# Kernel tuning notes

Measured on AMD Instinct MI355X. Metric: run time of the kernel, lower is better.

Reference implementation:

```python
import jax, jax.numpy as jnp
import numpy as np

NUM_HEADS = 8
HEAD_SPLITS = [2, 3, 3]          # heads per window size
WINDOWS = [3, 5, 7]


def _dwconv(x, w, b, k):
    """Depthwise 2D conv, SAME padding. x:[B,C,H,W], w:[C,1,k,k], b:[C]."""
    p = k // 2
    y = jax.lax.conv_general_dilated(
        x, w, window_strides=(1, 1), padding=[(p, p), (p, p)],
        dimension_numbers=("NCHW", "OIHW", "NCHW"),
        feature_group_count=x.shape[1])
    return y + b[None, :, None, None]


def setup_inputs() -> dict:
    key = jax.random.key(0)
    ks = jax.random.split(key, 8)
    B, N, C = 8, 3137, 768
    c = C // NUM_HEADS  # 96
    inp = {
        "x": jax.random.normal(ks[0], (B, N, C), dtype=jnp.float32),
        "qkv_w": jax.random.normal(ks[1], (3 * C, C), dtype=jnp.float32) * 0.02,
        "qkv_b": jnp.zeros((3 * C,), dtype=jnp.float32),
        "proj_w": jax.random.normal(ks[2], (C, C), dtype=jnp.float32) * 0.02,
        "proj_b": jnp.zeros((C,), dtype=jnp.float32),
        "conv3_w": jax.random.normal(ks[3], (2 * c, 1, 3, 3), dtype=jnp.float32) * 0.02,
        "conv3_b": jnp.zeros((2 * c,), dtype=jnp.float32),
        "conv5_w": jax.random.normal(ks[4], (3 * c, 1, 5, 5), dtype=jnp.float32) * 0.02,
        "conv5_b": jnp.zeros((3 * c,), dtype=jnp.float32),
        "conv7_w": jax.random.normal(ks[5], (3 * c, 1, 7, 7), dtype=jnp.float32) * 0.02,
        "conv7_b": jnp.zeros((3 * c,), dtype=jnp.float32),
        "H": 56,
        "W": 56,
    }
    return inp


def reference(x, qkv_w, qkv_b, proj_w, proj_b,
              conv3_w, conv3_b, conv5_w, conv5_b, conv7_w, conv7_b, H, W):
    B, N, C = x.shape
    h = NUM_HEADS
    c = C // h
    scale = c ** -0.5

    # qkv projection -> q,k,v each [B,h,N,c]
    qkv = x @ qkv_w.T + qkv_b
    qkv = qkv.reshape(B, N, 3, h, c).transpose(2, 0, 3, 1, 4)
    q, k, v = qkv[0], qkv[1], qkv[2]

    # factorized attention: softmax over token axis of k
    k_softmax = jax.nn.softmax(k, axis=2)
    kv = jnp.einsum("bhnc,bhnd->bhcd", k_softmax, v)       # [B,h,c,c]
    factor_att = jnp.einsum("bhnc,bhcd->bhnd", q, kv)      # [B,h,N,c]

    # ConvRelPosEnc on image tokens
    q_img = q[:, :, 1:, :]                                  # [B,h,HW,c]
    v_img = v[:, :, 1:, :]                                  # [B,h,HW,c]
    v_img = v_img.transpose(0, 1, 3, 2).reshape(B, h * c, H, W)
    splits = np.cumsum([s * c for s in HEAD_SPLITS])[:-1].tolist()
    v2, v5, v7 = jnp.split(v_img, splits, axis=1)
    conv_v = jnp.concatenate([
        _dwconv(v2, conv3_w, conv3_b, 3),
        _dwconv(v5, conv5_w, conv5_b, 5),
        _dwconv(v7, conv7_w, conv7_b, 7),
    ], axis=1)                                              # [B,h*c,H,W]
    conv_v = conv_v.reshape(B, h, c, H * W).transpose(0, 1, 3, 2)  # [B,h,HW,c]
    ev = q_img * conv_v
    crpe = jnp.pad(ev, ((0, 0), (0, 0), (1, 0), (0, 0)))    # zero row for cls token

    out = scale * factor_att + crpe                         # [B,h,N,c]
    out = out.transpose(0, 2, 1, 3).reshape(B, N, C)
    out = out @ proj_w.T + proj_b
    return out
```

## Files before the change

### kernel.cpp

```cpp
#include <hip/hip_runtime.h>
#include <hip/hip_bf16.h>


#define BB 8
#define NN 3137
#define HH 8
#define CH 96
#define HW 3136
#define IMG 56
#define MTOK (BB*NN)
#define NCHK 16
#define CTOK 197

typedef __bf16 bf16x8 __attribute__((ext_vector_type(8)));
typedef unsigned short u16x8 __attribute__((ext_vector_type(8)));
typedef unsigned short u16x4 __attribute__((ext_vector_type(4)));
typedef float  f32x4  __attribute__((ext_vector_type(4)));
typedef float  f32x8  __attribute__((ext_vector_type(8)));

__device__ __forceinline__ void gl_lds16(const void* g, void* l) {
    __builtin_amdgcn_global_load_lds(
        (const __attribute__((address_space(1))) unsigned int*)g,
        (__attribute__((address_space(3))) unsigned int*)l, 16, 0, 0);
}

__global__ __launch_bounds__(256) void cvt_bf16(
    const float* __restrict__ in, unsigned short* __restrict__ out, int n8)
{
    const int i = blockIdx.x * 256 + threadIdx.x;
    if (i < n8) {
        const f32x8 v = ((const f32x8*)in)[i];
        ((u16x8*)out)[i] = (u16x8)__builtin_convertvector(v, bf16x8);
    }
}

template<bool OUT_F32>
__global__ __launch_bounds__(256) void gemm_bt(
    const unsigned short* __restrict__ A, int lda,
    const unsigned short* __restrict__ W,
    const float* __restrict__ bias,
    void* __restrict__ Cptr, int ldc,
    int M, int Nd, int K)
{
    __shared__ alignas(16) unsigned short As[128*32];
    __shared__ alignas(16) unsigned short Bs[128*32];
    const int tid  = threadIdx.x;
    const int nwg = gridDim.x * gridDim.y;
    int orig = blockIdx.y * gridDim.x + blockIdx.x;
    const int q8 = nwg >> 3, r8 = nwg & 7;
    const int xcd = orig & 7, off = orig >> 3;
    const int wgid = (xcd < r8 ? xcd*(q8+1) : r8*(q8+1) + (xcd-r8)*q8) + off;
    const int n0   = (wgid % gridDim.x) * 128;
    const int m0   = (wgid / gridDim.x) * 128;
    const int lane = tid & 63;
    const int wave = tid >> 6;
    const int wm   = (wave >> 1) * 64;
    const int wn   = (wave & 1) * 64;
    const int lr   = lane & 15;
    const int quad = lane >> 4;

    const int r0 = tid >> 2, c0 = (tid & 3) * 8;
    const int r1 = r0 + 64;
    int am0 = m0 + r0; if (am0 > M-1) am0 = M-1;
    int am1 = m0 + r1; if (am1 > M-1) am1 = M-1;
    const unsigned short* a0 = A + (size_t)am0*lda + c0;
    const unsigned short* a1 = A + (size_t)am1*lda + c0;
    const unsigned short* w0 = W + (size_t)(n0+r0)*K + c0;
    const unsigned short* w1 = W + (size_t)(n0+r1)*K + c0;
    unsigned short* lA0 = As + tid*8;
    unsigned short* lA1 = As + (tid+256)*8;
    unsigned short* lB0 = Bs + tid*8;
    unsigned short* lB1 = Bs + (tid+256)*8;

    f32x4 acc[4][4] = {};
    for (int k0 = 0; k0 < K; k0 += 32) {
        __syncthreads();
        gl_lds16(a0 + k0, lA0);
        gl_lds16(a1 + k0, lA1);
        gl_lds16(w0 + k0, lB0);
        gl_lds16(w1 + k0, lB1);
        asm volatile("s_waitcnt vmcnt(0)" ::: "memory");
        __syncthreads();
        bf16x8 af[4], bfr[4];
#pragma unroll
        for (int i = 0; i < 4; ++i) {
            af[i]  = *(const bf16x8*)(As + (wm + i*16 + lr)*32 + quad*8);
            bfr[i] = *(const bf16x8*)(Bs + (wn + i*16 + lr)*32 + quad*8);
        }
#pragma unroll
        for (int i = 0; i < 4; ++i)
#pragma unroll
            for (int j = 0; j < 4; ++j)
                acc[i][j] = __builtin_amdgcn_mfma_f32_16x16x32_bf16(bfr[j], af[i], acc[i][j], 0, 0, 0);
    }
#pragma unroll
    for (int i = 0; i < 4; ++i) {
        const int row = m0 + wm + i*16 + lr;
        if (row < M) {
#pragma unroll
            for (int j = 0; j < 4; ++j) {
                const int col = n0 + wn + j*16 + quad*4;
                const f32x4 bv = *(const f32x4*)(bias + col);
                f32x4 v;
#pragma unroll
                for (int r = 0; r < 4; ++r) v[r] = acc[i][j][r] + bv[r];
                if (OUT_F32) {
                    *(f32x4*)&((float*)Cptr)[(size_t)row*ldc + col] = v;
                } else {
                    u16x4 st;
#pragma unroll
                    for (int r = 0; r < 4; ++r)
                        st[r] = __hip_bfloat16_raw(__float2bfloat16(v[r])).x;
                    *(u16x4*)&((__hip_bfloat16*)Cptr)[(size_t)row*ldc + col] = st;
                }
            }
        }
    }
}

__global__ __launch_bounds__(256) void kv_accum(
    const __hip_bfloat16* __restrict__ qkv,
    float* __restrict__ kvp,
    float* __restrict__ spart)
{
    const int bh = blockIdx.x;
    const int chunk = blockIdx.y;
    const int b = bh >> 3, h = bh & 7;
    const int nstart = chunk * CTOK;
    int nend = nstart + CTOK; if (nend > NN) nend = NN;
    __shared__ float krow[16][96], vrow[16][96];
    __shared__ float sacc[192][8];
    const int t = threadIdx.x;

    const int sr = t / 12, sc = (t % 12) * 8;
    const __hip_bfloat16* kb = qkv + (size_t)b*NN*2304 + 768 + h*96;
    const __hip_bfloat16* vb = kb + 768;
    float ssum[8] = {};

    const int ci = (t >> 4) * 6;
    const int di = (t & 15) * 6;
    float acc[6][6] = {};
    for (int n = nstart; n < nend; n += 16) {
        __syncthreads();
        if (t < 192) {
            const int nn = n + sr;
            if (nn < nend) {
                const bf16x8 kr = *(const bf16x8*)(kb + (size_t)nn*2304 + sc);
                const bf16x8 vr = *(const bf16x8*)(vb + (size_t)nn*2304 + sc);
                const f32x8 kf = __builtin_convertvector(kr, f32x8);
                const f32x8 vf = __builtin_convertvector(vr, f32x8);
                f32x8 ke;
#pragma unroll
                for (int j = 0; j < 8; ++j) { ke[j] = __expf(kf[j]); ssum[j] += ke[j]; }
                *(f32x4*)&krow[sr][sc]   = *(const f32x4*)&ke;
                *(f32x4*)&krow[sr][sc+4] = *((const f32x4*)&ke + 1);
                *(f32x4*)&vrow[sr][sc]   = *(const f32x4*)&vf;
                *(f32x4*)&vrow[sr][sc+4] = *((const f32x4*)&vf + 1);
            } else {
                const f32x4 z = {0.f,0.f,0.f,0.f};
                *(f32x4*)&krow[sr][sc] = z; *(f32x4*)&krow[sr][sc+4] = z;
                *(f32x4*)&vrow[sr][sc] = z; *(f32x4*)&vrow[sr][sc+4] = z;
            }
        }
        __syncthreads();
#pragma unroll 4
        for (int r = 0; r < 16; ++r) {
            float kf[6], vf[6];
#pragma unroll
            for (int i = 0; i < 6; ++i) kf[i] = krow[r][ci+i];
#pragma unroll
            for (int j = 0; j < 6; ++j) vf[j] = vrow[r][di+j];
#pragma unroll
            for (int i = 0; i < 6; ++i)
#pragma unroll
                for (int j = 0; j < 6; ++j)
                    acc[i][j] += kf[i] * vf[j];
        }
    }
    float* outp = kvp + (size_t)(chunk*64 + bh)*9216;
#pragma unroll
    for (int i = 0; i < 6; ++i)
#pragma unroll
        for (int j = 0; j < 6; ++j)
            outp[(ci+i)*96 + (di+j)] = acc[i][j];
    if (t < 192) {
#pragma unroll
        for (int j = 0; j < 8; ++j) sacc[t][j] = ssum[j];
    }
    __syncthreads();
    if (t < 96) {
        const int g = t >> 3, e = t & 7;
        float S = 0.f;
#pragma unroll
        for (int m = 0; m < 16; ++m) S += sacc[g + 12*m][e];
        spart[(size_t)(chunk*64 + bh)*96 + t] = S;
    }
}

__global__ __launch_bounds__(256) void kv_prep(
    const float* __restrict__ kvp, const float* __restrict__ spart,
    unsigned short* __restrict__ kvb)
{
    const int bh = blockIdx.x, y = blockIdx.y;
    __shared__ float sinv[24];
    const int t = threadIdx.x;
    const int cbase = y * 24;
    if (t < 24) {
        float S = 0.f;
#pragma unroll
        for (int ch = 0; ch < NCHK; ++ch)
            S += spart[(size_t)(ch*64 + bh)*96 + cbase + t];
        sinv[t] = 1.0f / S;
    }
    __syncthreads();
    unsigned short* dst = kvb + (size_t)bh*19968;
    for (int i = t; i < 2304; i += 256) {
        const int ii = y*2304 + i;
        const int c = ii / 96, d = ii % 96;
        float v = 0.f;
#pragma unroll
        for (int ch = 0; ch < NCHK; ++ch)
            v += kvp[(size_t)(ch*64 + bh)*9216 + ii];
        v *= sinv[c - cbase];
        const __hip_bfloat16 hb = __float2bfloat16(v);
        const float lo = v - __bfloat162float(hb);
        const __hip_bfloat16 lb = __float2bfloat16(lo);
        dst[d*104 + c]        = __hip_bfloat16_raw(hb).x;
        dst[9984 + d*104 + c] = __hip_bfloat16_raw(lb).x;
    }
}

__global__ __launch_bounds__(256) void fatt(
    const __hip_bfloat16* __restrict__ qkv,
    const unsigned short* __restrict__ kvb,
    const __hip_bfloat16* __restrict__ cv,
    __hip_bfloat16* __restrict__ att)
{
    __shared__ alignas(16) unsigned short kvs[2*96*104];
    const int tile = blockIdx.x, h = blockIdx.y, b = blockIdx.z;
    const int t = threadIdx.x, lane = t & 63, wave = t >> 6;
    const int lr = lane & 15, quad = lane >> 4;

    const unsigned short* kg = kvb + (size_t)(b*8 + h)*19968;
#pragma unroll
    for (int s = 0; s < 10; ++s) {
        const int slot = t + s*256;
        if (slot < 2496) gl_lds16(kg + slot*8, kvs + slot*8);
    }

    const int n0 = tile*128 + wave*32;
    const unsigned short* qbu = (const unsigned short*)qkv + (size_t)b*NN*2304 + h*96;
    bf16x8 af[2][3];
#pragma unroll
    for (int i = 0; i < 2; ++i) {
        int n = n0 + i*16 + lr; if (n > NN-1) n = NN-1;
#pragma unroll
        for (int kk = 0; kk < 3; ++kk)
            af[i][kk] = *(const bf16x8*)(qbu + (size_t)n*2304 + kk*32 + quad*8);
    }
    asm volatile("s_waitcnt vmcnt(0)" ::: "memory");
    __syncthreads();

    f32x4 acc[2][6] = {};
#pragma unroll
    for (int j = 0; j < 6; ++j) {
#pragma unroll
        for (int kk = 0; kk < 3; ++kk) {
            const bf16x8 bhh = *(const bf16x8*)(kvs + (j*16 + lr)*104 + kk*32 + quad*8);
            const bf16x8 bll = *(const bf16x8*)(kvs + 9984 + (j*16 + lr)*104 + kk*32 + quad*8);
#pragma unroll
            for (int i = 0; i < 2; ++i) {
                acc[i][j] = __builtin_amdgcn_mfma_f32_16x16x32_bf16(af[i][kk], bhh, acc[i][j], 0, 0, 0);
                acc[i][j] = __builtin_amdgcn_mfma_f32_16x16x32_bf16(af[i][kk], bll, acc[i][j], 0, 0, 0);
            }
        }
    }

    const float scale = 0.10206207261596577f;
    const __hip_bfloat16* qb  = (const __hip_bfloat16*)qbu;
    const __hip_bfloat16* cvb = cv + (size_t)(b*8 + h)*HW*96;
    __hip_bfloat16* ab = att + (size_t)b*NN*2304 + h*96;
#pragma unroll
    for (int i = 0; i < 2; ++i) {
#pragma unroll
        for (int j = 0; j < 6; ++j) {
            const int col = j*16 + lr;
#pragma unroll
            for (int r = 0; r < 4; ++r) {
                const int n = n0 + i*16 + quad*4 + r;
                if (n < NN) {
                    float v = scale * acc[i][j][r];
                    if (n > 0) {
                        const float qv = __bfloat162float(qb[(size_t)n*2304 + col]);
                        v += qv * __bfloat162float(cvb[(size_t)(n-1)*96 + col]);
                    }
                    ab[(size_t)n*2304 + col] = __float2bfloat16(v);
                }
            }
        }
    }
}

template<int KS>
__device__ __forceinline__ void dw_band(
    float (*vt)[64][36],
    const __hip_bfloat16* __restrict__ vbase,
    const float* __restrict__ wp, float bv,
    __hip_bfloat16* __restrict__ cvo,
    int y0)
{
    constexpr int P = KS/2;
    const int t = threadIdx.x;
    float wr[KS*KS];
#pragma unroll
    for (int i = 0; i < KS*KS; ++i) wr[i] = wp[i];

    const int spx = t >> 2, sc0 = (t & 3) * 8;
    const int ch = t & 31, xs = t >> 5;
    const int xbase = xs*7 + 4 - P;

#pragma unroll
    for (int r = -P; r < P; ++r) {
        const int y = y0 + r;
        if (t < 224) {
            f32x8 v8 = {0,0,0,0,0,0,0,0};
            if ((unsigned)y < (unsigned)IMG) {
                const bf16x8 rv = *(const bf16x8*)(vbase + (size_t)(y*IMG + spx)*2304 + sc0);
                v8 = __builtin_convertvector(rv, f32x8);
            }
            float* dst = &vt[(y+8)&7][spx+4][sc0];
            *(f32x4*)dst     = *(f32x4*)&v8;
            *(f32x4*)(dst+4) = *((f32x4*)&v8 + 1);
        }
    }

    for (int yy = y0; yy < y0 + 14; ++yy) {
        {
            const int y = yy + P;
            if (t < 224) {
                f32x8 v8 = {0,0,0,0,0,0,0,0};
                if ((unsigned)y < (unsigned)IMG) {
                    const bf16x8 rv = *(const bf16x8*)(vbase + (size_t)(y*IMG + spx)*2304 + sc0);
                    v8 = __builtin_convertvector(rv, f32x8);
                }
                float* dst = &vt[(y+8)&7][spx+4][sc0];
                *(f32x4*)dst     = *(f32x4*)&v8;
                *(f32x4*)(dst+4) = *((f32x4*)&v8 + 1);
            }
        }
        __syncthreads();
        float acc[7];
#pragma unroll
        for (int j = 0; j < 7; ++j) acc[j] = bv;
        for (int dy = 0; dy < KS; ++dy) {
            const float* rowp = &vt[(yy + dy - P + 8) & 7][0][ch] + xbase*36;
            float win[7 + 2*P];
#pragma unroll
            for (int i = 0; i < 7 + 2*P; ++i) win[i] = rowp[i*36];
#pragma unroll
            for (int dx = 0; dx < KS; ++dx)
#pragma unroll
                for (int j = 0; j < 7; ++j)
                    acc[j] += wr[dy*KS+dx] * win[j+dx];
        }
        const int p0 = yy*IMG + xs*7;
#pragma unroll
        for (int j = 0; j < 7; ++j)
            cvo[(size_t)(p0 + j)*96] = __float2bfloat16(acc[j]);
        __syncthreads();
    }
}

__global__ __launch_bounds__(256) void dwconv2(
    const __hip_bfloat16* __restrict__ qkv,
    const float* __restrict__ w3, const float* __restrict__ b3,
    const float* __restrict__ w5, const float* __restrict__ b5,
    const float* __restrict__ w7, const float* __restrict__ b7,
    __hip_bfloat16* __restrict__ cv)
{
    __shared__ float vt[8][64][36];
    const int band = blockIdx.x, grp = blockIdx.y, b = blockIdx.z;
    const int t = threadIdx.x;
    {
        const int s = t >> 5, i = t & 31;
        const int xi = i >> 2;
        const int xp = (xi < 4) ? xi : 56 + xi;
        const int c0 = (i & 3) * 8;
        const f32x4 z = {0.f, 0.f, 0.f, 0.f};
        *(f32x4*)&vt[s][xp][c0]     = z;
        *(f32x4*)&vt[s][xp][c0+4]   = z;
    }
    const int chbase = grp * 32;
    const int wg = chbase + (t & 31);
    const int h = wg / 96, d = wg % 96;
    const int y0 = band * 14;
    const __hip_bfloat16* vbase = qkv + (size_t)b*NN*2304 + 2304 + 1536 + chbase;
    __hip_bfloat16* cvo = cv + ((size_t)(b*8 + h)*HW)*96 + d;
    if (grp < 6)        dw_band<3>(vt, vbase, w3 + wg*9,        b3[wg],     cvo, y0);
    else if (grp < 15)  dw_band<5>(vt, vbase, w5 + (wg-192)*25, b5[wg-192], cvo, y0);
    else                dw_band<7>(vt, vbase, w7 + (wg-480)*49, b7[wg-480], cvo, y0);
}

extern "C" void kernel_launch(void* const* d_in, const int* in_sizes, int n_in,
                              void* d_out, int out_size, void* d_ws, size_t ws_size,
                              hipStream_t stream)
{
    const float* x      = (const float*)d_in[0];
    const float* qkv_w  = (const float*)d_in[1];
    const float* qkv_b  = (const float*)d_in[2];
    const float* proj_w = (const float*)d_in[3];
    const float* proj_b = (const float*)d_in[4];
    const float* w3 = (const float*)d_in[5];
    const float* b3 = (const float*)d_in[6];
    const float* w5 = (const float*)d_in[7];
    const float* b5 = (const float*)d_in[8];
    const float* w7 = (const float*)d_in[9];
    const float* b7 = (const float*)d_in[10];
    float* out = (float*)d_out;

    char* ws = (char*)d_ws;
    const size_t QKV_B = (size_t)MTOK * 2304 * 2;
    const size_t XB_B  = (size_t)MTOK * 768 * 2;
    const size_t SH_B  = XB_B;
    const size_t KV_B  = (size_t)64 * 9216 * 4;
    const size_t ST_B  = 49152;
    const size_t WB_B  = (size_t)2304 * 768 * 2;
    const size_t PW_B  = (size_t)768 * 768 * 2;
    if (ws_size < QKV_B + SH_B + KV_B + ST_B + WB_B + PW_B) return;
    __hip_bfloat16* qkv  = (__hip_bfloat16*)ws;
    unsigned short* xb   = (unsigned short*)(ws + QKV_B);
    float*          kvp  = (float*)(ws + QKV_B);
    float*          spart= (float*)(ws + QKV_B + (size_t)NCHK*64*9216*4);
    __hip_bfloat16* cv   = (__hip_bfloat16*)(ws + QKV_B);
    unsigned short* wb   = (unsigned short*)(ws + QKV_B + SH_B + KV_B + ST_B);
    unsigned short* pwb  = (unsigned short*)(ws + QKV_B + SH_B + KV_B + ST_B + WB_B);

    cvt_bf16<<<(MTOK*768/8 + 255)/256, 256, 0, stream>>>(x, xb, MTOK*768/8);
    cvt_bf16<<<(2304*768/8 + 255)/256, 256, 0, stream>>>(qkv_w, wb, 2304*768/8);
    cvt_bf16<<<(768*768/8 + 255)/256, 256, 0, stream>>>(proj_w, pwb, 768*768/8);
    gemm_bt<false><<<dim3(18, 197), 256, 0, stream>>>(
        xb, 768, wb, qkv_b, qkv, 2304, MTOK, 2304, 768);
    kv_accum<<<dim3(64, NCHK), 256, 0, stream>>>(qkv, kvp, spart);
    kv_prep<<<dim3(64, 4), 256, 0, stream>>>(kvp, spart, wb);
    dwconv2<<<dim3(4, 24, 8), 256, 0, stream>>>(qkv, w3, b3, w5, b5, w7, b7, cv);
    fatt<<<dim3(25, 8, 8), 256, 0, stream>>>(qkv, wb, cv,
                                             (__hip_bfloat16*)ws + 768);
    gemm_bt<true><<<dim3(6, 197), 256, 0, stream>>>(
        (const unsigned short*)ws + 768, 2304, pwb, proj_b, out, 768,
        MTOK, 768, 768);
}
```

Baseline: 514.6 us.

## Replace QKV GEMM with 256x256-tile pipelined MFMA kernel

```diff
diff --git a/kernel.cpp b/kernel.cpp
--- a/kernel.cpp
+++ b/kernel.cpp
@@ -23,6 +23,11 @@
         (const __attribute__((address_space(1))) unsigned int*)g,
         (__attribute__((address_space(3))) unsigned int*)l, 16, 0, 0);
 }
+__device__ __forceinline__ void memfence_bar() {
+    asm volatile("" ::: "memory");
+    __builtin_amdgcn_s_barrier();
+    asm volatile("" ::: "memory");
+}
 
 __global__ __launch_bounds__(256) void cvt_bf16(
     const float* __restrict__ in, unsigned short* __restrict__ out, int n8)
@@ -31,6 +36,120 @@
     if (i < n8) {
         const f32x8 v = ((const f32x8*)in)[i];
         ((u16x8*)out)[i] = (u16x8)__builtin_convertvector(v, bf16x8);
+    }
+}
+
+__global__ __launch_bounds__(512, 2) void gemm256(
+    const unsigned short* __restrict__ A,
+    const unsigned short* __restrict__ W,
+    const float* __restrict__ bias,
+    unsigned short* __restrict__ C,
+    int lda, int ldw, int ldc, int M, int NT)
+{
+    __shared__ alignas(16) unsigned short lds[2*2*2*8192];
+    const int tid = threadIdx.x;
+    const int nwg = gridDim.x * gridDim.y;
+    const int orig = blockIdx.y * gridDim.x + blockIdx.x;
+    const int q8 = nwg >> 3, r8 = nwg & 7;
+    const int xcd = orig & 7, off = orig >> 3;
+    const int wgid = (xcd < r8 ? xcd*(q8+1) : r8*(q8+1) + (xcd-r8)*q8) + off;
+    const int n0 = (wgid % gridDim.x) * 256;
+    const int m0 = (wgid / gridDim.x) * 256;
+
+    const int lane = tid & 63, wave = tid >> 6;
+    const int lr = lane & 15, quad = lane >> 4;
+    const int wm2 = wave >> 2;
+    const int wn4 = wave & 3;
+    const int bh  = wn4 >> 1;
+    const int brow = (wn4 & 1) * 64;
+
+    const int srow0 = tid >> 3, skc0 = tid & 7;
+    const int srow1 = (tid + 512) >> 3, skc1 = tid & 7;
+    const int kce0 = (skc0 ^ (srow0 & 7)) * 8;
+    const int kce1 = (skc1 ^ (srow1 & 7)) * 8;
+
+    auto stage = [&](int p, int mat, int h, int t) {
+        unsigned short* dst = lds + (((p*2 + mat)*2 + h) << 13);
+        const int kb = t * 64;
+        if (mat == 0) {
+            int g0 = m0 + h*128 + srow0; if (g0 > M-1) g0 = M-1;
+            int g1 = m0 + h*128 + srow1; if (g1 > M-1) g1 = M-1;
+            gl_lds16(A + (size_t)g0*lda + kb + kce0, dst + tid*8);
+            gl_lds16(A + (size_t)g1*lda + kb + kce1, dst + (tid+512)*8);
+        } else {
+            const int g0 = n0 + h*128 + srow0;
+            const int g1 = n0 + h*128 + srow1;
+            gl_lds16(W + (size_t)g0*ldw + kb + kce0, dst + tid*8);
+            gl_lds16(W + (size_t)g1*ldw + kb + kce1, dst + (tid+512)*8);
+        }
+    };
+    auto ldsrd = [&](const unsigned short* base, int rowh, int c16) -> bf16x8 {
+        return *(const bf16x8*)(base + rowh*64 + ((c16 ^ (rowh & 7)) << 3));
+    };
+
+    stage(0,1,0,0); stage(0,1,1,0);
+    stage(0,0,0,0); stage(0,0,1,0);
+    stage(1,1,0,1); stage(1,1,1,1);
+    asm volatile("s_waitcnt vmcnt(4)" ::: "memory");
+    memfence_bar();
+
+    f32x4 acc[8][4] = {};
+    bf16x8 bfr[4][2], af[2][2];
+    for (int t = 0; t < NT; ++t) {
+        const int p = t & 1;
+        const unsigned short* Abuf = lds + (((p*2 + 0)*2 + wm2) << 13);
+        const unsigned short* Bbuf = lds + (((p*2 + 1)*2 + bh ) << 13);
+#pragma unroll
+        for (int q = 0; q < 4; ++q) {
+            if (q == 0) {
+#pragma unroll
+                for (int j = 0; j < 4; ++j)
+#pragma unroll
+                    for (int ks = 0; ks < 2; ++ks)
+                        bfr[j][ks] = ldsrd(Bbuf, brow + j*16 + lr, ks*4 + quad);
+            }
+#pragma unroll
+            for (int ii = 0; ii < 2; ++ii)
+#pragma unroll
+                for (int ks = 0; ks < 2; ++ks)
+                    af[ii][ks] = ldsrd(Abuf, q*32 + ii*16 + lr, ks*4 + quad);
+            if (q == 0) { if (t+1 < NT) stage(p^1, 0, 0, t+1); }
+            else if (q == 1) { if (t+1 < NT) stage(p^1, 0, 1, t+1); }
+            else if (q == 2) { if (t+2 < NT) stage(p, 1, 0, t+2); }
+            else             { if (t+2 < NT) stage(p, 1, 1, t+2); }
+            __builtin_amdgcn_s_setprio(1);
+#pragma unroll
+            for (int ii = 0; ii < 2; ++ii)
+#pragma unroll
+                for (int j = 0; j < 4; ++j)
+#pragma unroll
+                    for (int ks = 0; ks < 2; ++ks)
+                        acc[q*2+ii][j] = __builtin_amdgcn_mfma_f32_16x16x32_bf16(
+                            bfr[j][ks], af[ii][ks], acc[q*2+ii][j], 0, 0, 0);
+            __builtin_amdgcn_s_setprio(0);
+            if (q == 3) {
+                if (t+2 < NT)      asm volatile("s_waitcnt vmcnt(4)" ::: "memory");
+                else if (t+1 < NT) asm volatile("s_waitcnt vmcnt(0)" ::: "memory");
+            }
+            memfence_bar();
+        }
+    }
+
+#pragma unroll
+    for (int i = 0; i < 8; ++i) {
+        const int row = m0 + wm2*128 + i*16 + lr;
+        if (row < M) {
+#pragma unroll
+            for (int j = 0; j < 4; ++j) {
+                const int col = n0 + wn4*64 + j*16 + quad*4;
+                const f32x4 bv = *(const f32x4*)(bias + col);
+                u16x4 st;
+#pragma unroll
+                for (int r = 0; r < 4; ++r)
+                    st[r] = __hip_bfloat16_raw(__float2bfloat16(acc[i][j][r] + bv[r])).x;
+                *(u16x4*)&C[(size_t)row*ldc + col] = st;
+            }
+        }
     }
 }
 
@@ -438,8 +557,8 @@
     cvt_bf16<<<(MTOK*768/8 + 255)/256, 256, 0, stream>>>(x, xb, MTOK*768/8);
     cvt_bf16<<<(2304*768/8 + 255)/256, 256, 0, stream>>>(qkv_w, wb, 2304*768/8);
     cvt_bf16<<<(768*768/8 + 255)/256, 256, 0, stream>>>(proj_w, pwb, 768*768/8);
-    gemm_bt<false><<<dim3(18, 197), 256, 0, stream>>>(
-        xb, 768, wb, qkv_b, qkv, 2304, MTOK, 2304, 768);
+    gemm256<<<dim3(9, 99), 512, 0, stream>>>(
+        xb, wb, qkv_b, (unsigned short*)qkv, 768, 768, 2304, MTOK, 768/64);
     kv_accum<<<dim3(64, NCHK), 256, 0, stream>>>(qkv, kvp, spart);
     kv_prep<<<dim3(64, 4), 256, 0, stream>>>(kvp, spart, wb);
     dwconv2<<<dim3(4, 24, 8), 256, 0, stream>>>(qkv, w3, b3, w5, b5, w7, b7, cv);
```

Result: no change. 509.0 us (-1.1%).
